# Kernel tuning notes

Hardware: AMD Instinct MI355X
Metric: run time of the kernel (lower is better)

Reference implementation:

```python
import jax, jax.numpy as jnp
import numpy as np

B, C, CK, HW = 4, 512, 512, 64
EPS = 1e-5


def conv1x1(x, w, b):
    # 1x1 conv == per-pixel linear: x [b,c,h,w], w [o,c], b [o]
    return jnp.einsum('bchw,oc->bohw', x, w) + b[None, :, None, None]


def mean_variance_norm(feat):
    # torch .var(dim=2) defaults to unbiased (ddof=1)
    b, c = feat.shape[:2]
    flat = feat.reshape(b, c, -1)
    mean = flat.mean(axis=-1)
    std = jnp.sqrt(flat.var(axis=-1, ddof=1) + EPS)
    return (feat - mean[:, :, None, None]) / std[:, :, None, None]


def setup_inputs() -> dict:
    key = jax.random.key(0)
    ks = jax.random.split(key, 10)
    sc_k = 1.0 / np.sqrt(CK)
    sc_c = 1.0 / np.sqrt(C)
    return {
        'content': jax.random.normal(ks[0], (B, C, HW, HW), jnp.float32),
        'style': jax.random.normal(ks[1], (B, C, HW, HW), jnp.float32),
        'content_key': jax.random.normal(ks[2], (B, CK, HW, HW), jnp.float32),
        'style_key': jax.random.normal(ks[3], (B, CK, HW, HW), jnp.float32),
        'f_w': jax.random.normal(ks[4], (CK, CK), jnp.float32) * sc_k,
        'f_b': jnp.zeros((CK,), jnp.float32),
        'g_w': jax.random.normal(ks[5], (CK, CK), jnp.float32) * sc_k,
        'g_b': jnp.zeros((CK,), jnp.float32),
        'h_w': jax.random.normal(ks[6], (C, C), jnp.float32) * sc_c,
        'h_b': jnp.zeros((C,), jnp.float32),
        'w_mix': jnp.ones((2,), jnp.float32),
    }


def reference(content, style, content_key, style_key,
              f_w, f_b, g_w, g_b, h_w, h_b, w_mix):
    Fm = conv1x1(content_key, f_w, f_b)   # [b,ck,h,w]
    Gm = conv1x1(style_key, g_w, g_b)     # [b,ck,hs,ws]
    Hm = conv1x1(style, h_w, h_b)         # [b,c,hs,ws]
    b, ck, h, w = Fm.shape
    c = Hm.shape[1]

    G = Gm.reshape(b, ck, -1)                                # [b,ck,Ns]
    style_flat = Hm.reshape(b, c, -1).transpose(0, 2, 1)      # [b,Ns,c]
    Fq = Fm.reshape(b, ck, -1).transpose(0, 2, 1)             # [b,Nc,ck]

    raw_attn = jnp.einsum('bnk,bkm->bnm', Fq, G)              # [b,Nc,Ns]
    attn_dense = jax.nn.softmax(raw_attn, axis=-1)
    attn_sparse = jax.nn.softmax(jax.nn.relu(raw_attn), axis=-1)

    wts = jax.nn.softmax(w_mix)  # exp(w)/sum(exp(w))
    S = jax.nn.softmax(attn_dense * wts[0] + attn_sparse * wts[1], axis=-1)

    mean = jnp.einsum('bnm,bmc->bnc', S, style_flat)          # E[x]
    second = jnp.einsum('bnm,bmc->bnc', S, style_flat ** 2)   # E[x^2]
    std = jnp.sqrt(jax.nn.relu(second - mean ** 2))

    mean = mean.reshape(b, h, w, c).transpose(0, 3, 1, 2)
    std = std.reshape(b, h, w, c).transpose(0, 3, 1, 2)
    return std * mean_variance_norm(content) + mean
```

## Files before the change

kernel.cpp:

```cpp
#include <hip/hip_runtime.h>
#include <hip/hip_bf16.h>
#include <hip/hip_fp16.h>
#include <stdint.h>

typedef float f32x4 __attribute__((ext_vector_type(4)));
typedef short short8 __attribute__((ext_vector_type(8)));
typedef unsigned short ushort4_t __attribute__((ext_vector_type(4)));
typedef unsigned short u16;

#if defined(__has_builtin)
#if __has_builtin(__builtin_amdgcn_exp2f)
#define EXP2(x) __builtin_amdgcn_exp2f(x)
#else
#define EXP2(x) exp2f(x)
#endif
#else
#define EXP2(x) exp2f(x)
#endif

static __device__ __forceinline__ u16 f2bf(float f) {
    __hip_bfloat16 h = __float2bfloat16(f);
    return *reinterpret_cast<const u16*>(&h);
}
static __device__ __forceinline__ u16 f2h(float f) {
    __half h = __float2half(f);
    return *reinterpret_cast<const u16*>(&h);
}
static __device__ __forceinline__ float h2f(u16 b) {
    __half h = *reinterpret_cast<const __half*>(&b);
    return __half2float(h);
}

static __device__ __forceinline__ void gload16(const void* g, void* l) {
    __builtin_amdgcn_global_load_lds((const __attribute__((address_space(1))) void*)g,
                                     (__attribute__((address_space(3))) void*)l, 16, 0, 0);
}

__global__ void k_cast3(const float* __restrict__ a, const float* __restrict__ b,
                        const float* __restrict__ c, u16* __restrict__ oa,
                        u16* __restrict__ ob, u16* __restrict__ oc) {
    int i = blockIdx.x * blockDim.x + threadIdx.x;
    int which = i >> 16, j = i & 65535;
    const float* in = (which == 0) ? a : (which == 1) ? b : c;
    u16* out = (which == 0) ? oa : (which == 1) ? ob : oc;
    float4 v = ((const float4*)in)[j];
    ushort4 o;
    o.x = f2bf(v.x); o.y = f2bf(v.y); o.z = f2bf(v.z); o.w = f2bf(v.w);
    ((ushort4*)out)[j] = o;
}

__global__ __launch_bounds__(256) void k_transpose(const float* __restrict__ in, u16* __restrict__ out) {
    __shared__ float t[64][65];
    int b = blockIdx.z;
    int c0 = blockIdx.y * 64;
    int n0 = blockIdx.x * 64;
    const float* ip = in + ((size_t)b * 512 + c0) * 4096 + n0;
#pragma unroll
    for (int i = 0; i < 16; ++i) {
        int idx = threadIdx.x + i * 256;
        int cl = idx >> 6, nl = idx & 63;
        t[cl][nl] = ip[(size_t)cl * 4096 + nl];
    }
    __syncthreads();
    u16* op = out + ((size_t)b * 4096 + n0) * 512 + c0;
#pragma unroll
    for (int i = 0; i < 16; ++i) {
        int idx = threadIdx.x + i * 256;
        int nr = idx >> 6, cc = idx & 63;
        op[(size_t)nr * 512 + cc] = f2bf(t[cc][nr]);
    }
}

__global__ __launch_bounds__(256) void k_cstats(const float* __restrict__ content, float* __restrict__ cstat) {
    int c = blockIdx.x, b = blockIdx.y;
    const float4* r4 = (const float4*)(content + ((size_t)b * 512 + c) * 4096);
    float s = 0.f, ss = 0.f;
    for (int i = threadIdx.x; i < 1024; i += 256) {
        float4 v = r4[i];
        s += v.x + v.y + v.z + v.w;
        ss += v.x * v.x + v.y * v.y + v.z * v.z + v.w * v.w;
    }
#pragma unroll
    for (int k = 1; k < 64; k <<= 1) { s += __shfl_xor(s, k); ss += __shfl_xor(ss, k); }
    __shared__ float ls[4], lss[4];
    int w = threadIdx.x >> 6;
    if ((threadIdx.x & 63) == 0) { ls[w] = s; lss[w] = ss; }
    __syncthreads();
    if (threadIdx.x == 0) {
        s = ls[0] + ls[1] + ls[2] + ls[3];
        ss = lss[0] + lss[1] + lss[2] + lss[3];
        float mu = s / 4096.f;
        float var = (ss - 4096.f * mu * mu) / 4095.f;
        cstat[((size_t)b * 512 + c) * 2] = mu;
        cstat[((size_t)b * 512 + c) * 2 + 1] = rsqrtf(var + 1e-5f);
    }
}

__global__ __launch_bounds__(256) void k_convP(const u16* __restrict__ XT, const u16* __restrict__ Wb,
                                               const float* __restrict__ bias, u16* __restrict__ out) {
    int bid = blockIdx.x;
    int b = (bid & 7) >> 1;
    int u = ((bid & 1) << 8) | (bid >> 3);
    int n0 = (u & 63) * 64, o0 = (u >> 6) * 64;
    int lane = threadIdx.x & 63, w = threadIdx.x >> 6;
    int l15 = lane & 15, l4 = lane >> 4;
    const u16* ap = XT + ((size_t)b * 4096 + n0 + w * 16 + l15) * 512 + l4 * 8;
    f32x4 acc[4] = {{0,0,0,0},{0,0,0,0},{0,0,0,0},{0,0,0,0}};
#pragma unroll
    for (int kk = 0; kk < 16; ++kk) {
        short8 a = *(const short8*)(ap + kk * 32);
#pragma unroll
        for (int bo = 0; bo < 4; ++bo) {
            const u16* bp = Wb + ((size_t)(o0 + bo * 16 + l15)) * 512 + kk * 32 + l4 * 8;
            short8 bb = *(const short8*)bp;
            acc[bo] = __builtin_amdgcn_mfma_f32_16x16x32_bf16(a, bb, acc[bo], 0, 0, 0);
        }
    }
#pragma unroll
    for (int bo = 0; bo < 4; ++bo) {
        float bv = bias[o0 + bo * 16 + l15];
#pragma unroll
        for (int r = 0; r < 4; ++r) {
            int n = n0 + w * 16 + l4 * 4 + r;
            out[((size_t)b * 4096 + n) * 512 + o0 + bo * 16 + l15] = f2bf(acc[bo][r] + bv);
        }
    }
}

__global__ __launch_bounds__(256) void k_convH(const u16* __restrict__ ST, const u16* __restrict__ Wb,
                                               const float* __restrict__ bias, u16* __restrict__ out) {
    int bid = blockIdx.x;
    int b = (bid & 7) >> 1;
    int u = ((bid & 1) << 8) | (bid >> 3);
    int m0 = (u & 63) * 64, o0 = (u >> 6) * 64;
    int lane = threadIdx.x & 63, w = threadIdx.x >> 6;
    int l15 = lane & 15, l4 = lane >> 4;
    const u16* ap = Wb + ((size_t)(o0 + w * 16 + l15)) * 512 + l4 * 8;
    f32x4 acc[4] = {{0,0,0,0},{0,0,0,0},{0,0,0,0},{0,0,0,0}};
#pragma unroll
    for (int kk = 0; kk < 16; ++kk) {
        short8 a = *(const short8*)(ap + kk * 32);
#pragma unroll
        for (int mb = 0; mb < 4; ++mb) {
            const u16* bp = ST + ((size_t)b * 4096 + m0 + mb * 16 + l15) * 512 + kk * 32 + l4 * 8;
            short8 bb = *(const short8*)bp;
            acc[mb] = __builtin_amdgcn_mfma_f32_16x16x32_bf16(a, bb, acc[mb], 0, 0, 0);
        }
    }
#pragma unroll
    for (int r = 0; r < 4; ++r) {
        int o = o0 + w * 16 + l4 * 4 + r;
        float bv = bias[o];
#pragma unroll
        for (int mb = 0; mb < 4; ++mb) {
            float v = acc[mb][r] + bv;
            size_t base = ((size_t)b * 1024 + o) * 4096 + m0 + mb * 16 + l15;
            out[base] = f2bf(v);
            out[base + (size_t)512 * 4096] = f2bf(v * v);
        }
    }
}

__global__ __launch_bounds__(512, 4) void k_attnA(
    const u16* __restrict__ Q, const u16* __restrict__ G,
    u16* __restrict__ Lg, float* __restrict__ stats) {

    __shared__ __align__(16) u16 gtile[2][32 * 512];
    __shared__ float smd[4][2][16], ssd_[4][2][16], smsp[4][2][16], sssp[4][2][16];

    int bid = blockIdx.x;
    int b = (bid & 7) >> 1;
    int half = bid & 1;
    int qt = bid >> 3;
    int n0 = qt * 64;
    int kv0 = half * 2048;
    int lane = threadIdx.x & 63, w = threadIdx.x >> 6;
    int l15 = lane & 15, l4 = lane >> 4;
    int R = w >> 1, MB = w & 1;
    const float L2E = 1.44269504f;

    const u16* qp = Q + ((size_t)b * 4096 + n0 + R * 16 + l15) * 512 + l4 * 8;
    short8 q[16];
#pragma unroll
    for (int kk = 0; kk < 16; ++kk) q[kk] = *(const short8*)(qp + kk * 32);

    const char* gbat = (const char*)(G + (size_t)b * 4096 * 512);
    size_t lgoff = ((size_t)b * 4096 + n0 + R * 16 + l15) * 4096 + kv0 + MB * 16 + l4 * 4;

#define STAGEA(buf, mc)                                                                \
    {                                                                                  \
        _Pragma("unroll")                                                              \
        for (int j = 0; j < 4; ++j) {                                                  \
            int row = j * 8 + w;                                                       \
            const char* src = gbat + ((size_t)(kv0 + (mc) * 32 + row)) * 1024          \
                              + ((lane * 16) ^ ((row & 7) << 4));                      \
            gload16(src, (char*)&gtile[buf][0] + row * 1024);                          \
        }                                                                              \
    }

    float md = -1e30f, sd = 0.f, ms = -1e30f, ss = 0.f;

    STAGEA(0, 0);
    __syncthreads();
    for (int mc = 0; mc < 64; ++mc) {
        int buf = mc & 1;
        if (mc < 63) STAGEA(buf ^ 1, mc + 1);
        f32x4 acc = {0, 0, 0, 0};
        const char* gt = (const char*)&gtile[buf][0];
        int row = MB * 16 + l15;
#pragma unroll
        for (int kk = 0; kk < 16; ++kk) {
            int y = (kk * 64 + l4 * 16) ^ ((row & 7) << 4);
            short8 gg = *(const short8*)(gt + row * 1024 + y);
            acc = __builtin_amdgcn_mfma_f32_16x16x32_bf16(gg, q[kk], acc, 0, 0, 0);
        }
        float v0 = acc[0], v1 = acc[1], v2 = acc[2], v3 = acc[3];
        float mx = fmaxf(fmaxf(v0, v1), fmaxf(v2, v3));
        float mn = fmaxf(md, mx);
        sd = sd * __expf(md - mn) +
             ((__expf(v0 - mn) + __expf(v1 - mn)) + (__expf(v2 - mn) + __expf(v3 - mn)));
        md = mn;
        float mns = fmaxf(ms, fmaxf(mx, 0.f));
        ss = ss * __expf(ms - mns) +
             ((__expf(fmaxf(v0, 0.f) - mns) + __expf(fmaxf(v1, 0.f) - mns)) +
              (__expf(fmaxf(v2, 0.f) - mns) + __expf(fmaxf(v3, 0.f) - mns)));
        ms = mns;
        ushort4_t pk = {f2h(v0 * L2E), f2h(v1 * L2E), f2h(v2 * L2E), f2h(v3 * L2E)};
        *(ushort4_t*)(Lg + lgoff + (size_t)mc * 32) = pk;
        __syncthreads();
    }

#pragma unroll
    for (int k = 16; k < 64; k <<= 1) {
        float mo = __shfl_xor(md, k), so = __shfl_xor(sd, k);
        float mn = fmaxf(md, mo);
        sd = sd * __expf(md - mn) + so * __expf(mo - mn);
        md = mn;
        mo = __shfl_xor(ms, k); so = __shfl_xor(ss, k);
        mn = fmaxf(ms, mo);
        ss = ss * __expf(ms - mn) + so * __expf(mo - mn);
        ms = mn;
    }
    if (l4 == 0) {
        smd[R][MB][l15] = md; ssd_[R][MB][l15] = sd;
        smsp[R][MB][l15] = ms; sssp[R][MB][l15] = ss;
    }
    __syncthreads();
    if (MB == 0 && lane < 16) {
        float m0_ = smd[R][0][l15], s0_ = ssd_[R][0][l15];
        float m1_ = smd[R][1][l15], s1_ = ssd_[R][1][l15];
        float mn = fmaxf(m0_, m1_);
        float Sd = s0_ * __expf(m0_ - mn) + s1_ * __expf(m1_ - mn);
        float Md = mn;
        m0_ = smsp[R][0][l15]; s0_ = sssp[R][0][l15];
        m1_ = smsp[R][1][l15]; s1_ = sssp[R][1][l15];
        mn = fmaxf(m0_, m1_);
        float Ss = s0_ * __expf(m0_ - mn) + s1_ * __expf(m1_ - mn);
        float Ms = mn;
        int qg = n0 + R * 16 + l15;
        float4 st = {Md, Sd, Ms, Ss};
        *(float4*)(stats + (((size_t)b * 4096 + qg) * 2 + half) * 4) = st;
    }
#undef STAGEA
}

__global__ __launch_bounds__(1024, 1) void k_attnB(
    const u16* __restrict__ Lg, const u16* __restrict__ H,
    const float* __restrict__ stats, const float* __restrict__ wmix,
    const float* __restrict__ content, const float* __restrict__ cstat,
    float* __restrict__ out) {

    __shared__ __align__(16) u16 et[2][8192];
    __shared__ float zrow[128];

    int bid = blockIdx.x;
    int b = (bid & 7) >> 1;
    int qt = ((bid & 1) << 4) | (bid >> 4);
    int cs = (bid >> 3) & 1;
    int n0 = qt * 128;
    int tid = threadIdx.x;
    int lane = tid & 63, w = tid >> 6;
    int l15 = lane & 15, l4 = lane >> 4;
    int qh = w & 1, chw = w >> 1;

    const float L2E = 1.44269504f;
    float wa = wmix[0], wbv = wmix[1];
    float wmx = fmaxf(wa, wbv);
    float e0 = __expf(wa - wmx), e1 = __expf(wbv - wmx);
    float w0l = e0 / (e0 + e1) * L2E, w1l = e1 / (e0 + e1) * L2E;

    int prow = tid >> 3;
    int kvb = (tid & 7) * 8;
    float md2, ms2;
    {
        const float* sp = stats + (((size_t)b * 4096 + n0 + prow) * 2) * 4;
        float4 s0 = *(const float4*)sp;
        float4 s1 = *(const float4*)(sp + 4);
        float mn = fmaxf(s0.x, s1.x);
        float S = s0.y * __expf(s0.x - mn) + s1.y * __expf(s1.x - mn);
        md2 = mn * L2E + __log2f(S);
        mn = fmaxf(s0.z, s1.z);
        S = s0.w * __expf(s0.z - mn) + s1.w * __expf(s1.z - mn);
        ms2 = mn * L2E + __log2f(S);
    }
    const u16* lgrow = Lg + ((size_t)b * 4096 + n0 + prow) * 4096 + kvb;
    unsigned ewbyte = (unsigned)(prow * 128) +
                      (((unsigned)(tid & 7) * 16) ^ ((unsigned)(prow & 7) << 4));
    float z = 0.f;

#define PRODUCE(ebase, LV)                                                             \
    {                                                                                  \
        short8 L8 = (LV);                                                              \
        short8 ebf;                                                                    \
        float za = 0.f, zb = 0.f;                                                      \
        _Pragma("unroll")                                                              \
        for (int j = 0; j < 8; ++j) {                                                  \
            float t = h2f((u16)L8[j]);                                                 \
            float ed = EXP2(t - md2);                                                  \
            float es = EXP2(fmaxf(t, 0.f) - ms2);                                      \
            float e = EXP2(fmaf(w0l, ed, w1l * es));                                   \
            if (j & 1) zb += e; else za += e;                                          \
            ebf[j] = (short)f2bf(e);                                                   \
        }                                                                              \
        z += za + zb;                                                                  \
        *(short8*)((char*)(ebase) + ewbyte) = ebf;                                     \
    }

    f32x4 pv[16];
#pragma unroll
    for (int i = 0; i < 16; ++i) pv[i] = (f32x4){0, 0, 0, 0};

    short8 Lcur = *(const short8*)(lgrow);
    PRODUCE(&et[0][0], Lcur);
    short8 Lnext = *(const short8*)(lgrow + 64);
    __syncthreads();

    for (int mc = 0; mc < 64; ++mc) {
        int buf = mc & 1;
        if (mc < 63) {
            short8 Lp = Lnext;
            if (mc < 62) Lnext = *(const short8*)(lgrow + (size_t)(mc + 2) * 64);
            PRODUCE(&et[buf ^ 1][0], Lp);
        }
        const char* eb = (const char*)&et[buf][0];
        const u16* hb = H + (size_t)b * 1024 * 4096 + (size_t)mc * 64 + l4 * 8;
#pragma unroll
        for (int ks = 0; ks < 2; ++ks) {
            short8 af[4];
#pragma unroll
            for (int qf = 0; qf < 4; ++qf) {
                int qq = qh * 64 + qf * 16 + l15;
                int y = (ks * 64 + l4 * 16) ^ ((qq & 7) << 4);
                af[qf] = *(const short8*)(eb + qq * 128 + y);
            }
            __builtin_amdgcn_s_setprio(1);
#pragma unroll
            for (int cf = 0; cf < 4; ++cf) {
                int c = (cf < 2) ? (cs * 256 + chw * 32 + cf * 16 + l15)
                                 : (512 + cs * 256 + chw * 32 + (cf - 2) * 16 + l15);
                short8 hh = *(const short8*)(hb + (size_t)c * 4096 + ks * 32);
#pragma unroll
                for (int qf = 0; qf < 4; ++qf)
                    pv[qf * 4 + cf] = __builtin_amdgcn_mfma_f32_16x16x32_bf16(af[qf], hh, pv[qf * 4 + cf], 0, 0, 0);
            }
            __builtin_amdgcn_s_setprio(0);
        }
        __syncthreads();
    }

    z += __shfl_xor(z, 1);
    z += __shfl_xor(z, 2);
    z += __shfl_xor(z, 4);
    if ((tid & 7) == 0) zrow[prow] = z;
    __syncthreads();

#pragma unroll
    for (int qf = 0; qf < 4; ++qf) {
        float iz[4];
#pragma unroll
        for (int r = 0; r < 4; ++r)
            iz[r] = 1.f / zrow[qh * 64 + qf * 16 + l4 * 4 + r];
#pragma unroll
        for (int cf = 0; cf < 2; ++cf) {
            int c = cs * 256 + chw * 32 + cf * 16 + l15;
            float mu = cstat[((size_t)b * 512 + c) * 2];
            float rstd = cstat[((size_t)b * 512 + c) * 2 + 1];
            const float* cp = content + ((size_t)b * 512 + c) * 4096 + n0 + qh * 64 + qf * 16 + l4 * 4;
            float* op = out + ((size_t)b * 512 + c) * 4096 + n0 + qh * 64 + qf * 16 + l4 * 4;
            float4 cv = *(const float4*)cp;
            float4 ov;
#pragma unroll
            for (int r = 0; r < 4; ++r) {
                float mean = pv[qf * 4 + cf][r] * iz[r];
                float sec = pv[qf * 4 + cf + 2][r] * iz[r];
                float stdv = sqrtf(fmaxf(sec - mean * mean, 0.f));
                (&ov.x)[r] = stdv * ((&cv.x)[r] - mu) * rstd + mean;
            }
            *(float4*)op = ov;
        }
    }
#undef PRODUCE
}

extern "C" void kernel_launch(void* const* d_in, const int* in_sizes, int n_in,
                              void* d_out, int out_size, void* d_ws, size_t ws_size,
                              hipStream_t stream) {
    (void)in_sizes; (void)n_in; (void)out_size; (void)ws_size;
    const float* content = (const float*)d_in[0];
    const float* style   = (const float*)d_in[1];
    const float* ckey    = (const float*)d_in[2];
    const float* skey    = (const float*)d_in[3];
    const float* f_w = (const float*)d_in[4];
    const float* f_b = (const float*)d_in[5];
    const float* g_w = (const float*)d_in[6];
    const float* g_b = (const float*)d_in[7];
    const float* h_w = (const float*)d_in[8];
    const float* h_b = (const float*)d_in[9];
    const float* wmix = (const float*)d_in[10];
    float* out = (float*)d_out;

    const size_t MiB = 1048576;
    char* ws = (char*)d_ws;
    u16* ckT = (u16*)(ws + 0);
    u16* skT = (u16*)(ws + 16 * MiB);
    u16* stT = (u16*)(ws + 32 * MiB);
    u16* fwB = (u16*)(ws + 48 * MiB);
    u16* gwB = (u16*)(ws + 48 * MiB + 524288);
    u16* hwB = (u16*)(ws + 49 * MiB);
    float* cst = (float*)(ws + 49 * MiB + 524288);
    u16* Qb  = (u16*)(ws + 50 * MiB);
    u16* Gb  = (u16*)(ws + 66 * MiB);
    u16* Hb  = (u16*)(ws + 0);
    u16* Lg  = (u16*)(ws + 82 * MiB);
    float* stats = (float*)(ws + 210 * MiB);

    k_cast3<<<768, 256, 0, stream>>>(f_w, g_w, h_w, fwB, gwB, hwB);
    k_transpose<<<dim3(64, 8, 4), 256, 0, stream>>>(ckey, ckT);
    k_transpose<<<dim3(64, 8, 4), 256, 0, stream>>>(skey, skT);
    k_transpose<<<dim3(64, 8, 4), 256, 0, stream>>>(style, stT);
    k_cstats<<<dim3(512, 4), 256, 0, stream>>>(content, cst);
    k_convP<<<dim3(2048), 256, 0, stream>>>(ckT, fwB, f_b, Qb);
    k_convP<<<dim3(2048), 256, 0, stream>>>(skT, gwB, g_b, Gb);
    k_convH<<<dim3(2048), 256, 0, stream>>>(stT, hwB, h_b, Hb);
    k_attnA<<<dim3(512), 512, 0, stream>>>(Qb, Gb, Lg, stats);
    k_attnB<<<dim3(256), 1024, 0, stream>>>(Lg, Hb, stats, wmix, content, cst, out);
}
```

Before: 811.0 us.

## Stage H tiles into double-buffered LDS via async loads, single-buffer exp tile

```diff
diff --git a/kernel.cpp b/kernel.cpp
--- a/kernel.cpp
+++ b/kernel.cpp
@@ -270,7 +270,8 @@
     const float* __restrict__ content, const float* __restrict__ cstat,
     float* __restrict__ out) {
 
-    __shared__ __align__(16) u16 et[2][8192];
+    __shared__ __align__(16) u16 ht[2][512 * 64];
+    __shared__ __align__(16) u16 et[8192];
     __shared__ float zrow[128];
 
     int bid = blockIdx.x;
@@ -308,7 +309,20 @@
                       (((unsigned)(tid & 7) * 16) ^ ((unsigned)(prow & 7) << 4));
     float z = 0.f;
 
-#define PRODUCE(ebase, LV)                                                             \
+    const char* hbat = (const char*)(H + (size_t)b * 1024 * 4096);
+#define STAGEH(buf, mc)                                                                \
+    {                                                                                  \
+        _Pragma("unroll")                                                              \
+        for (int j = 0; j < 4; ++j) {                                                  \
+            int row = w * 32 + j * 8 + (lane >> 3);                                    \
+            int c = (row < 256) ? (cs * 256 + row) : (512 + cs * 256 + (row - 256));   \
+            const char* src = hbat + (size_t)c * 8192 + (size_t)(mc) * 128             \
+                              + ((((lane & 7) * 16)) ^ ((row & 7) << 4));              \
+            gload16(src, (char*)&ht[buf][0] + (w * 32 + j * 8) * 128);                 \
+        }                                                                              \
+    }
+
+#define PRODUCE(LV)                                                                    \
     {                                                                                  \
         short8 L8 = (LV);                                                              \
         short8 ebf;                                                                    \
@@ -323,27 +337,30 @@
             ebf[j] = (short)f2bf(e);                                                   \
         }                                                                              \
         z += za + zb;                                                                  \
-        *(short8*)((char*)(ebase) + ewbyte) = ebf;                                     \
+        *(short8*)((char*)&et[0] + ewbyte) = ebf;                                      \
     }
 
     f32x4 pv[16];
 #pragma unroll
     for (int i = 0; i < 16; ++i) pv[i] = (f32x4){0, 0, 0, 0};
 
+    STAGEH(0, 0);
     short8 Lcur = *(const short8*)(lgrow);
-    PRODUCE(&et[0][0], Lcur);
     short8 Lnext = *(const short8*)(lgrow + 64);
     __syncthreads();
 
     for (int mc = 0; mc < 64; ++mc) {
         int buf = mc & 1;
-        if (mc < 63) {
-            short8 Lp = Lnext;
-            if (mc < 62) Lnext = *(const short8*)(lgrow + (size_t)(mc + 2) * 64);
-            PRODUCE(&et[buf ^ 1][0], Lp);
-        }
-        const char* eb = (const char*)&et[buf][0];
-        const u16* hb = H + (size_t)b * 1024 * 4096 + (size_t)mc * 64 + l4 * 8;
+        if (mc < 63) STAGEH(buf ^ 1, mc + 1);
+        PRODUCE(Lcur);
+        Lcur = Lnext;
+        if (mc < 62) Lnext = *(const short8*)(lgrow + (size_t)(mc + 2) * 64);
+
+        asm volatile("s_waitcnt lgkmcnt(0)" ::: "memory");
+        __builtin_amdgcn_s_barrier();
+        __builtin_amdgcn_sched_barrier(0);
+
+        const char* hb = (const char*)&ht[buf][0];
 #pragma unroll
         for (int ks = 0; ks < 2; ++ks) {
             short8 af[4];
@@ -351,14 +368,15 @@
             for (int qf = 0; qf < 4; ++qf) {
                 int qq = qh * 64 + qf * 16 + l15;
                 int y = (ks * 64 + l4 * 16) ^ ((qq & 7) << 4);
-                af[qf] = *(const short8*)(eb + qq * 128 + y);
+                af[qf] = *(const short8*)((const char*)&et[0] + qq * 128 + y);
             }
             __builtin_amdgcn_s_setprio(1);
 #pragma unroll
             for (int cf = 0; cf < 4; ++cf) {
-                int c = (cf < 2) ? (cs * 256 + chw * 32 + cf * 16 + l15)
-                                 : (512 + cs * 256 + chw * 32 + (cf - 2) * 16 + l15);
-                short8 hh = *(const short8*)(hb + (size_t)c * 4096 + ks * 32);
+                int row = (cf < 2) ? (chw * 32 + cf * 16 + l15)
+                                   : (256 + chw * 32 + (cf - 2) * 16 + l15);
+                int y = (ks * 64 + l4 * 16) ^ ((row & 7) << 4);
+                short8 hh = *(const short8*)(hb + row * 128 + y);
 #pragma unroll
                 for (int qf = 0; qf < 4; ++qf)
                     pv[qf * 4 + cf] = __builtin_amdgcn_mfma_f32_16x16x32_bf16(af[qf], hh, pv[qf * 4 + cf], 0, 0, 0);
@@ -400,6 +418,7 @@
         }
     }
 #undef PRODUCE
+#undef STAGEH
 }
 
 extern "C" void kernel_launch(void* const* d_in, const int* in_sizes, int n_in,
```

Result: faster. 673.5 us (-17.0%).
